# Kernel optimization log

Hardware: AMD Instinct MI355X
Metric: run time of the kernel (lower is better)

## Reference

```python
import jax, jax.numpy as jnp
import numpy as np

N = 500000   # pins
E = 2000000  # cell edges (avg fan-in ~4)
D = 64       # in_feats_dim == out_feats_dim
DC = 64      # cell_feat_dim
HID = 256    # MLP hidden (hardcoded in MLP)
T = 100000   # target nodes


def _mlp(x, W1, b1, W2, b2):
    # nn.Sequential(Linear, ReLU, Linear); dropout declared but unused
    return jax.nn.relu(x @ W1 + b1) @ W2 + b2


def setup_inputs() -> dict:
    key = jax.random.key(0)
    ks = jax.random.split(key, 14)
    s = lambda d: np.float32(1.0 / np.sqrt(d))
    return {
        "h": jax.random.normal(ks[0], (N, D), jnp.float32),
        "cell_feat": jax.random.normal(ks[1], (N, DC), jnp.float32),
        "attn": jax.random.normal(ks[2], (1, 1, D), jnp.float32) * s(D),
        "Wn1": jax.random.normal(ks[3], (D, HID), jnp.float32) * s(D),
        "bn1": jnp.zeros((HID,), jnp.float32),
        "Wn2": jax.random.normal(ks[4], (HID, D), jnp.float32) * s(HID),
        "bn2": jnp.zeros((D,), jnp.float32),
        "Ws1": jax.random.normal(ks[5], (DC, HID), jnp.float32) * s(DC),
        "bs1": jnp.zeros((HID,), jnp.float32),
        "Ws2": jax.random.normal(ks[6], (HID, D), jnp.float32) * s(HID),
        "bs2": jnp.zeros((D,), jnp.float32),
        "src": jax.random.randint(ks[7], (E,), 0, N, jnp.int32),
        "dst": jax.random.randint(ks[8], (E,), 0, N, jnp.int32),
        "targets": jax.random.randint(ks[9], (T,), 0, N, jnp.int32),
    }


def reference(h, cell_feat, attn, Wn1, bn1, Wn2, bn2, Ws1, bs1, Ws2, bs2,
              src, dst, targets):
    # --- cal_edge_attn: e = relu((h_src * attn).sum(-1)), shape [E, heads=1]
    h_src = h[src]                                        # [E, D]
    e = jax.nn.relu(jnp.einsum("ed,hd->eh", h_src, attn[0]))  # [E, 1]
    # --- th.sparse.softmax(sp, 0): segment softmax over edges per dst node
    m = jax.ops.segment_max(e, dst, num_segments=N)       # [N, 1]
    m = jnp.where(jnp.isfinite(m), m, jnp.float32(0.0))   # empty segments
    ex = jnp.exp(e - m[dst])                              # [E, 1]
    denom = jax.ops.segment_sum(ex, dst, num_segments=N)  # [N, 1]
    a = ex / denom[dst]                                   # [E, 1]
    # --- pull: fn.u_mul_e('h','a','m') + fn.sum -> h_neigh1
    h_neigh1 = jax.ops.segment_sum(h_src * a, dst, num_segments=N)  # [N, D]
    # --- apply_cell_func: fc_cell_self(cell_feat) + fc_cell_neigh(h_neigh1)
    h_out = _mlp(cell_feat, Ws1, bs1, Ws2, bs2) + _mlp(h_neigh1, Wn1, bn1, Wn2, bn2)
    # --- trailing activation (relu)
    h_out = jax.nn.relu(h_out)
    return h_out[targets]
```

## Files before the change

### kernel.cpp

```cpp
#include <hip/hip_runtime.h>
#include <stdint.h>

#define CAP 32

typedef short bf16x8 __attribute__((ext_vector_type(8)));
typedef short bf16x4 __attribute__((ext_vector_type(4)));
typedef float f32x4  __attribute__((ext_vector_type(4)));

__device__ __forceinline__ unsigned short f2bf(float f) {
    unsigned u = __float_as_uint(f);
    unsigned r = u + 0x7fffu + ((u >> 16) & 1u);
    return (unsigned short)(r >> 16);
}

__global__ __launch_bounds__(256) void k_flag_prep(
    const int* __restrict__ targets, int* __restrict__ slotmap,
    int* __restrict__ count, int T,
    const float* __restrict__ Wn1, const float* __restrict__ Ws1,
    const float* __restrict__ Wn2, const float* __restrict__ Ws2,
    short* __restrict__ W1sw, short* __restrict__ W2sw)
{
    int t = blockIdx.x * blockDim.x + threadIdx.x;
    if (t < 4096) {
        int lane = t & 63;
        int kt = (t >> 6) & 1;
        int nt = (t >> 7) & 15;
        int s  = (t >> 11) & 1;
        const float* W = s ? Ws1 : Wn1;
        int col = nt * 16 + (lane & 15);
        int krow = kt * 32 + (lane >> 4) * 8;
        bf16x8 v;
#pragma unroll
        for (int j = 0; j < 8; j++)
            v[j] = (short)f2bf(W[(size_t)(krow + j) * 256 + col]);
        ((bf16x8*)W1sw)[t] = v;
    } else if (t < 8192) {
        int u = t - 4096;
        int lane = u & 63;
        int kt = (u >> 6) & 7;
        int nt = (u >> 9) & 3;
        int s  = (u >> 11) & 1;
        const float* W = s ? Ws2 : Wn2;
        int col = nt * 16 + (lane & 15);
        int krow = kt * 32 + (lane >> 4) * 8;
        bf16x8 v;
#pragma unroll
        for (int j = 0; j < 8; j++)
            v[j] = (short)f2bf(W[(size_t)(krow + j) * 64 + col]);
        ((bf16x8*)W2sw)[u] = v;
    }
    if (t < T) {
        int g = targets[t];
        int old = atomicCAS(&slotmap[g], -1, -2);
        if (old == -1) {
            int u = atomicAdd(count, 1) + 1;
            slotmap[g] = u;
        }
    }
}

__global__ __launch_bounds__(256) void k_scatter(
    const int* __restrict__ src, const int* __restrict__ dst,
    const int* __restrict__ slotmap, int* __restrict__ cnt,
    int* __restrict__ esrc, int E)
{
    int e = blockIdx.x * blockDim.x + threadIdx.x;
    if (e >= E) return;
    int d = dst[e];
    int sl = slotmap[d];
    if (sl < 0) return;
    int pos = atomicAdd(&cnt[sl], 1) + 1;
    if (pos < CAP) esrc[sl * CAP + pos] = src[e];
}

__global__ __launch_bounds__(256) void k_gather(
    const float* __restrict__ h, const float* __restrict__ attn,
    const int* __restrict__ cnt, const int* __restrict__ esrc,
    short* __restrict__ hncb, int T)
{
    int tid = blockIdx.x * blockDim.x + threadIdx.x;
    int gid = tid >> 4;
    int lane = tid & 15;
    if (gid >= T) return;
    int n = cnt[gid] + 1;
    if (n > CAP) n = CAP;
    int base = gid * CAP;
    int idx = esrc[base + lane];
    float4 av = *(const float4*)(attn + lane * 4);
    float m = 0.f, den = 0.f;
    float4 o = make_float4(0.f, 0.f, 0.f, 0.f);
    if (n > 0) {
        int s0 = __shfl(idx, 0, 16);
        float4 hv = *(const float4*)(h + (size_t)s0 * 64 + lane * 4);
        for (int j = 0; j < n; j++) {
            float4 hn = hv;
            if (j + 1 < n) {
                int s1 = (j + 1 < 16) ? __shfl(idx, j + 1, 16) : esrc[base + j + 1];
                hn = *(const float4*)(h + (size_t)s1 * 64 + lane * 4);
            }
            float p = hv.x * av.x + hv.y * av.y + hv.z * av.z + hv.w * av.w;
            p += __shfl_xor(p, 1);
            p += __shfl_xor(p, 2);
            p += __shfl_xor(p, 4);
            p += __shfl_xor(p, 8);
            float e = fmaxf(p, 0.f);
            float mn = fmaxf(m, e);
            float corr = __expf(m - mn);
            float w = __expf(e - mn);
            den = den * corr + w;
            o.x = o.x * corr + w * hv.x;
            o.y = o.y * corr + w * hv.y;
            o.z = o.z * corr + w * hv.z;
            o.w = o.w * corr + w * hv.w;
            m = mn;
            hv = hn;
        }
    }
    bf16x4 pk = (bf16x4){0, 0, 0, 0};
    if (n > 0) {
        float inv = 1.f / den;
        pk[0] = (short)f2bf(o.x * inv);
        pk[1] = (short)f2bf(o.y * inv);
        pk[2] = (short)f2bf(o.z * inv);
        pk[3] = (short)f2bf(o.w * inv);
    }
    *(bf16x4*)(hncb + (size_t)gid * 64 + lane * 4) = pk;
}

__global__ __launch_bounds__(128, 4) void k_mlp_mfma(
    const short* __restrict__ hncb, const int* __restrict__ slotmap,
    const float* __restrict__ cf,
    const short* __restrict__ W1sw, const short* __restrict__ W2sw,
    const float* __restrict__ bn1, const float* __restrict__ bs1,
    const float* __restrict__ bn2, const float* __restrict__ bs2,
    const int* __restrict__ targets, float* __restrict__ out, int T)
{
    __shared__ short Hlds[2][4096];
    const int tid = threadIdx.x;
    const int wave = tid >> 6, lane = tid & 63;
    const int m = lane & 15, quad = lane >> 4;
    const int mu = m & 7;
    const int rowbase = blockIdx.x * 32 + wave * 16;

    int grow = rowbase + m;
    int gi = (grow < T) ? grow : (T - 1);
    int g = targets[gi];
    bf16x8 bx[2][2];
    {
        int sl = slotmap[g];
        const short* hr = hncb + (size_t)sl * 64 + quad * 8;
        bx[0][0] = *(const bf16x8*)(hr);
        bx[0][1] = *(const bf16x8*)(hr + 32);
#pragma unroll
        for (int kt = 0; kt < 2; kt++) {
            const float* p = cf + (size_t)g * 64 + kt * 32 + quad * 8;
            f32x4 v0 = *(const f32x4*)p;
            f32x4 v1 = *(const f32x4*)(p + 4);
            bf16x8 t;
            t[0] = (short)f2bf(v0[0]); t[1] = (short)f2bf(v0[1]);
            t[2] = (short)f2bf(v0[2]); t[3] = (short)f2bf(v0[3]);
            t[4] = (short)f2bf(v1[0]); t[5] = (short)f2bf(v1[1]);
            t[6] = (short)f2bf(v1[2]); t[7] = (short)f2bf(v1[3]);
            bx[1][kt] = t;
        }
    }

    short* hb = &Hlds[wave][0];
    const bf16x8* W1f = (const bf16x8*)W1sw;
    const bf16x8* W2f = (const bf16x8*)W2sw;
    f32x4 acc2[4];
#pragma unroll
    for (int i = 0; i < 4; i++) acc2[i] = (f32x4){0.f, 0.f, 0.f, 0.f};

#define PF(buf, gidx) do { \
    buf[0] = Wp[(2 * (gidx)) * 128 + lane]; \
    buf[1] = Wp[(2 * (gidx)) * 128 + 64 + lane]; \
    buf[2] = Wp[(2 * (gidx) + 1) * 128 + lane]; \
    buf[3] = Wp[(2 * (gidx) + 1) * 128 + 64 + lane]; \
} while (0)

#define L1ONE(f0, f1, ntv) do { \
    const int nt_ = (ntv); \
    f32x4 a_ = {0.f, 0.f, 0.f, 0.f}; \
    a_ = __builtin_amdgcn_mfma_f32_16x16x32_bf16(f0, bx[s][0], a_, 0, 0, 0); \
    a_ = __builtin_amdgcn_mfma_f32_16x16x32_bf16(f1, bx[s][1], a_, 0, 0, 0); \
    f32x4 bias_ = *(const f32x4*)(b1 + nt_ * 16 + quad * 4); \
    bf16x4 pk_; \
    pk_[0] = (short)f2bf(fmaxf(a_[0] + bias_[0], 0.f)); \
    pk_[1] = (short)f2bf(fmaxf(a_[1] + bias_[1], 0.f)); \
    pk_[2] = (short)f2bf(fmaxf(a_[2] + bias_[2], 0.f)); \
    pk_[3] = (short)f2bf(fmaxf(a_[3] + bias_[3], 0.f)); \
    int G_ = 2 * nt_ + (quad >> 1); \
    *(bf16x4*)(hb + m * 256 + ((G_ ^ mu) << 3) + ((quad & 1) << 2)) = pk_; \
} while (0)

#define L1G(buf, gidx) do { \
    L1ONE(buf[0], buf[1], 2 * (gidx)); \
    L1ONE(buf[2], buf[3], 2 * (gidx) + 1); \
} while (0)

#pragma unroll
    for (int s = 0; s < 2; s++) {
        const float* b1 = s ? bs1 : bn1;
        const bf16x8* Wp = W1f + s * 2048;
        bf16x8 fA[4], fB[4];
        PF(fA, 0);
        PF(fB, 1); L1G(fA, 0);
        PF(fA, 2); L1G(fB, 1);
        PF(fB, 3); L1G(fA, 2);
        PF(fA, 4); L1G(fB, 3);
        PF(fB, 5); L1G(fA, 4);
        PF(fA, 6); L1G(fB, 5);
        PF(fB, 7); L1G(fA, 6);
        L1G(fB, 7);
#pragma unroll
        for (int nt2 = 0; nt2 < 4; nt2++) {
#pragma unroll
            for (int kt = 0; kt < 8; kt++) {
                bf16x8 af = *(const bf16x8*)(hb + m * 256 + (((4 * kt + quad) ^ mu) << 3));
                bf16x8 bw = W2f[(size_t)((s * 4 + nt2) * 8 + kt) * 64 + lane];
                acc2[nt2] = __builtin_amdgcn_mfma_f32_16x16x32_bf16(af, bw, acc2[nt2], 0, 0, 0);
            }
        }
    }
#undef PF
#undef L1ONE
#undef L1G

#pragma unroll
    for (int nt2 = 0; nt2 < 4; nt2++) {
        int j = nt2 * 16 + m;
        float b2 = bn2[j] + bs2[j];
#pragma unroll
        for (int r = 0; r < 4; r++) {
            int row = rowbase + quad * 4 + r;
            if (row < T) out[(size_t)row * 64 + j] = fmaxf(acc2[nt2][r] + b2, 0.f);
        }
    }
}

extern "C" void kernel_launch(void* const* d_in, const int* in_sizes, int n_in,
                              void* d_out, int out_size, void* d_ws, size_t ws_size,
                              hipStream_t stream)
{
    const float* h    = (const float*)d_in[0];
    const float* cf   = (const float*)d_in[1];
    const float* attn = (const float*)d_in[2];
    const float* Wn1  = (const float*)d_in[3];
    const float* bn1  = (const float*)d_in[4];
    const float* Wn2  = (const float*)d_in[5];
    const float* bn2  = (const float*)d_in[6];
    const float* Ws1  = (const float*)d_in[7];
    const float* bs1  = (const float*)d_in[8];
    const float* Ws2  = (const float*)d_in[9];
    const float* bs2  = (const float*)d_in[10];
    const int* src     = (const int*)d_in[11];
    const int* dst     = (const int*)d_in[12];
    const int* targets = (const int*)d_in[13];
    const int N = in_sizes[0] / 64;
    const int E = in_sizes[11];
    const int T = in_sizes[13];

    char* ws = (char*)d_ws;
    size_t off = 0;
    auto alloc = [&](size_t bytes) { size_t p = off; off = (off + bytes + 63) & ~(size_t)63; return p; };
    size_t o_hnc     = alloc((size_t)T * 64 * 2);
    size_t o_slotmap = alloc((size_t)N * 4);
    size_t o_cnt     = alloc((size_t)T * 4);
    size_t o_count   = alloc(4);
    size_t o_esrc    = alloc((size_t)T * CAP * 4);
    size_t o_w1      = alloc(32768 * 2);
    size_t o_w2      = alloc(32768 * 2);
    (void)o_w2;

    short* hncb   = (short*)(ws + o_hnc);
    int* slotmap  = (int*)(ws + o_slotmap);
    int* cnt      = (int*)(ws + o_cnt);
    int* count    = (int*)(ws + o_count);
    int* esrc     = (int*)(ws + o_esrc);
    short* W1sw   = (short*)(ws + o_w1);
    short* W2sw   = (short*)(ws + o_w2);

    (void)hipMemsetAsync(slotmap, 0xFF, (o_count + 4) - o_slotmap, stream);

    k_flag_prep<<<(T + 255) / 256, 256, 0, stream>>>(
        targets, slotmap, count, T, Wn1, Ws1, Wn2, Ws2, W1sw, W2sw);

    k_scatter<<<(E + 255) / 256, 256, 0, stream>>>(src, dst, slotmap, cnt, esrc, E);

    {
        long long thr = (long long)T * 16;
        k_gather<<<(unsigned)((thr + 255) / 256), 256, 0, stream>>>(
            h, attn, cnt, esrc, hncb, T);
    }

    k_mlp_mfma<<<(T + 31) / 32, 128, 0, stream>>>(
        hncb, slotmap, cf, W1sw, W2sw, bn1, bs1, bn2, bs2,
        targets, (float*)d_out, T);
}
```

Before: 389.5 us.

## Process two 16-row groups per wave in MLP kernel to reuse weight fragments

Each wave in the MFMA MLP kernel now handles 32 rows (two 16-row groups) instead of 16, so every loaded W1/W2 fragment feeds two MFMAs. This halves the global/L2 weight traffic per row and halves the block count. In exchange it doubles LDS per block and raises register use, with launch bounds relaxed to 2 blocks per CU, which lowers occupancy. It also moves the esrc index load in the gather kernel inside the n>0 branch to skip it for empty targets.

```diff
diff --git a/kernel.cpp b/kernel.cpp
--- a/kernel.cpp
+++ b/kernel.cpp
@@ -85,11 +85,11 @@
     int n = cnt[gid] + 1;
     if (n > CAP) n = CAP;
     int base = gid * CAP;
-    int idx = esrc[base + lane];
     float4 av = *(const float4*)(attn + lane * 4);
     float m = 0.f, den = 0.f;
     float4 o = make_float4(0.f, 0.f, 0.f, 0.f);
     if (n > 0) {
+        int idx = esrc[base + lane];
         int s0 = __shfl(idx, 0, 16);
         float4 hv = *(const float4*)(h + (size_t)s0 * 64 + lane * 4);
         for (int j = 0; j < n; j++) {
@@ -127,7 +127,7 @@
     *(bf16x4*)(hncb + (size_t)gid * 64 + lane * 4) = pk;
 }
 
-__global__ __launch_bounds__(128, 4) void k_mlp_mfma(
+__global__ __launch_bounds__(128, 2) void k_mlp_mfma(
     const short* __restrict__ hncb, const int* __restrict__ slotmap,
     const float* __restrict__ cf,
     const short* __restrict__ W1sw, const short* __restrict__ W2sw,
@@ -135,22 +135,23 @@
     const float* __restrict__ bn2, const float* __restrict__ bs2,
     const int* __restrict__ targets, float* __restrict__ out, int T)
 {
-    __shared__ short Hlds[2][4096];
+    __shared__ short Hlds[2][2][4096];
     const int tid = threadIdx.x;
     const int wave = tid >> 6, lane = tid & 63;
     const int m = lane & 15, quad = lane >> 4;
     const int mu = m & 7;
-    const int rowbase = blockIdx.x * 32 + wave * 16;
-
-    int grow = rowbase + m;
-    int gi = (grow < T) ? grow : (T - 1);
-    int g = targets[gi];
-    bf16x8 bx[2][2];
-    {
+    const int rowbase = blockIdx.x * 64 + wave * 32;
+
+    bf16x8 bx[2][2][2];
+#pragma unroll
+    for (int rg = 0; rg < 2; rg++) {
+        int grow = rowbase + rg * 16 + m;
+        int gi = (grow < T) ? grow : (T - 1);
+        int g = targets[gi];
         int sl = slotmap[g];
         const short* hr = hncb + (size_t)sl * 64 + quad * 8;
-        bx[0][0] = *(const bf16x8*)(hr);
-        bx[0][1] = *(const bf16x8*)(hr + 32);
+        bx[rg][0][0] = *(const bf16x8*)(hr);
+        bx[rg][0][1] = *(const bf16x8*)(hr + 32);
 #pragma unroll
         for (int kt = 0; kt < 2; kt++) {
             const float* p = cf + (size_t)g * 64 + kt * 32 + quad * 8;
@@ -161,16 +162,19 @@
             t[2] = (short)f2bf(v0[2]); t[3] = (short)f2bf(v0[3]);
             t[4] = (short)f2bf(v1[0]); t[5] = (short)f2bf(v1[1]);
             t[6] = (short)f2bf(v1[2]); t[7] = (short)f2bf(v1[3]);
-            bx[1][kt] = t;
-        }
-    }
-
-    short* hb = &Hlds[wave][0];
+            bx[rg][1][kt] = t;
+        }
+    }
+
+    short* hb0 = &Hlds[wave][0][0];
+    short* hb1 = &Hlds[wave][1][0];
     const bf16x8* W1f = (const bf16x8*)W1sw;
     const bf16x8* W2f = (const bf16x8*)W2sw;
-    f32x4 acc2[4];
-#pragma unroll
-    for (int i = 0; i < 4; i++) acc2[i] = (f32x4){0.f, 0.f, 0.f, 0.f};
+    f32x4 acc2[2][4];
+#pragma unroll
+    for (int rg = 0; rg < 2; rg++)
+#pragma unroll
+        for (int i = 0; i < 4; i++) acc2[rg][i] = (f32x4){0.f, 0.f, 0.f, 0.f};
 
 #define PF(buf, gidx) do { \
     buf[0] = Wp[(2 * (gidx)) * 128 + lane]; \
@@ -181,17 +185,26 @@
 
 #define L1ONE(f0, f1, ntv) do { \
     const int nt_ = (ntv); \
-    f32x4 a_ = {0.f, 0.f, 0.f, 0.f}; \
-    a_ = __builtin_amdgcn_mfma_f32_16x16x32_bf16(f0, bx[s][0], a_, 0, 0, 0); \
-    a_ = __builtin_amdgcn_mfma_f32_16x16x32_bf16(f1, bx[s][1], a_, 0, 0, 0); \
+    f32x4 a0_ = {0.f, 0.f, 0.f, 0.f}; \
+    f32x4 a1_ = {0.f, 0.f, 0.f, 0.f}; \
+    a0_ = __builtin_amdgcn_mfma_f32_16x16x32_bf16(f0, bx[0][s][0], a0_, 0, 0, 0); \
+    a0_ = __builtin_amdgcn_mfma_f32_16x16x32_bf16(f1, bx[0][s][1], a0_, 0, 0, 0); \
+    a1_ = __builtin_amdgcn_mfma_f32_16x16x32_bf16(f0, bx[1][s][0], a1_, 0, 0, 0); \
+    a1_ = __builtin_amdgcn_mfma_f32_16x16x32_bf16(f1, bx[1][s][1], a1_, 0, 0, 0); \
     f32x4 bias_ = *(const f32x4*)(b1 + nt_ * 16 + quad * 4); \
-    bf16x4 pk_; \
-    pk_[0] = (short)f2bf(fmaxf(a_[0] + bias_[0], 0.f)); \
-    pk_[1] = (short)f2bf(fmaxf(a_[1] + bias_[1], 0.f)); \
-    pk_[2] = (short)f2bf(fmaxf(a_[2] + bias_[2], 0.f)); \
-    pk_[3] = (short)f2bf(fmaxf(a_[3] + bias_[3], 0.f)); \
     int G_ = 2 * nt_ + (quad >> 1); \
-    *(bf16x4*)(hb + m * 256 + ((G_ ^ mu) << 3) + ((quad & 1) << 2)) = pk_; \
+    int off_ = m * 256 + ((G_ ^ mu) << 3) + ((quad & 1) << 2); \
+    bf16x4 pk0_, pk1_; \
+    pk0_[0] = (short)f2bf(fmaxf(a0_[0] + bias_[0], 0.f)); \
+    pk0_[1] = (short)f2bf(fmaxf(a0_[1] + bias_[1], 0.f)); \
+    pk0_[2] = (short)f2bf(fmaxf(a0_[2] + bias_[2], 0.f)); \
+    pk0_[3] = (short)f2bf(fmaxf(a0_[3] + bias_[3], 0.f)); \
+    pk1_[0] = (short)f2bf(fmaxf(a1_[0] + bias_[0], 0.f)); \
+    pk1_[1] = (short)f2bf(fmaxf(a1_[1] + bias_[1], 0.f)); \
+    pk1_[2] = (short)f2bf(fmaxf(a1_[2] + bias_[2], 0.f)); \
+    pk1_[3] = (short)f2bf(fmaxf(a1_[3] + bias_[3], 0.f)); \
+    *(bf16x4*)(hb0 + off_) = pk0_; \
+    *(bf16x4*)(hb1 + off_) = pk1_; \
 } while (0)
 
 #define L1G(buf, gidx) do { \
@@ -217,9 +230,12 @@
         for (int nt2 = 0; nt2 < 4; nt2++) {
 #pragma unroll
             for (int kt = 0; kt < 8; kt++) {
-                bf16x8 af = *(const bf16x8*)(hb + m * 256 + (((4 * kt + quad) ^ mu) << 3));
+                int hoff = m * 256 + (((4 * kt + quad) ^ mu) << 3);
                 bf16x8 bw = W2f[(size_t)((s * 4 + nt2) * 8 + kt) * 64 + lane];
-                acc2[nt2] = __builtin_amdgcn_mfma_f32_16x16x32_bf16(af, bw, acc2[nt2], 0, 0, 0);
+                bf16x8 af0 = *(const bf16x8*)(hb0 + hoff);
+                bf16x8 af1 = *(const bf16x8*)(hb1 + hoff);
+                acc2[0][nt2] = __builtin_amdgcn_mfma_f32_16x16x32_bf16(af0, bw, acc2[0][nt2], 0, 0, 0);
+                acc2[1][nt2] = __builtin_amdgcn_mfma_f32_16x16x32_bf16(af1, bw, acc2[1][nt2], 0, 0, 0);
             }
         }
     }
@@ -232,9 +248,12 @@
         int j = nt2 * 16 + m;
         float b2 = bn2[j] + bs2[j];
 #pragma unroll
-        for (int r = 0; r < 4; r++) {
-            int row = rowbase + quad * 4 + r;
-            if (row < T) out[(size_t)row * 64 + j] = fmaxf(acc2[nt2][r] + b2, 0.f);
+        for (int rg = 0; rg < 2; rg++) {
+#pragma unroll
+            for (int r = 0; r < 4; r++) {
+                int row = rowbase + rg * 16 + quad * 4 + r;
+                if (row < T) out[(size_t)row * 64 + j] = fmaxf(acc2[rg][nt2][r] + b2, 0.f);
+            }
         }
     }
 }
@@ -294,7 +313,7 @@
             h, attn, cnt, esrc, hncb, T);
     }
 
-    k_mlp_mfma<<<(T + 31) / 32, 128, 0, stream>>>(
+    k_mlp_mfma<<<(T + 63) / 64, 128, 0, stream>>>(
         hncb, slotmap, cf, W1sw, W2sw, bn1, bs1, bn2, bs2,
         targets, (float*)d_out, T);
 }
```

Result: no change. 394.7 us (+1.3%).
